# Kernel optimization log

Measured on AMD Instinct MI355X. Metric: run time of the kernel, lower is better.

The kernel has to match this reference:

```python
import jax, jax.numpy as jnp
import numpy as np

NUM_CLASSES = 2
THRESHOLD = 0.5
NEGPOS_RATIO = 3
VAR0, VAR1 = 0.1, 0.2  # self.variance = [0.1, 0.2]


def point_form(priors):
    # [cx,cy,w,h] -> [xmin,ymin,xmax,ymax]
    return jnp.concatenate([priors[:, :2] - priors[:, 2:] / 2,
                            priors[:, :2] + priors[:, 2:] / 2], axis=1)


def jaccard(a, b):
    # a: [O,4], b: [P,4] point-form -> IoU [O,P]
    tl = jnp.maximum(a[:, None, :2], b[None, :, :2])
    br = jnp.minimum(a[:, None, 2:], b[None, :, 2:])
    wh = jnp.clip(br - tl, 0.0)
    inter = wh[..., 0] * wh[..., 1]
    area_a = ((a[:, 2] - a[:, 0]) * (a[:, 3] - a[:, 1]))[:, None]
    area_b = ((b[:, 2] - b[:, 0]) * (b[:, 3] - b[:, 1]))[None, :]
    return inter / (area_a + area_b - inter)


def encode(matched, priors):
    # matched: [P,4] point-form GT, priors: [P,4] center-size
    g_cxcy = ((matched[:, :2] + matched[:, 2:]) / 2 - priors[:, :2]) / (VAR0 * priors[:, 2:])
    g_wh = jnp.log((matched[:, 2:] - matched[:, :2]) / priors[:, 2:]) / VAR1
    return jnp.concatenate([g_cxcy, g_wh], axis=1)


def match_one(truths, labels, priors):
    # truths: [O,4], labels: [O], priors: [P,4]
    O = truths.shape[0]
    overlaps = jaccard(truths, point_form(priors))          # [O,P]
    best_prior_idx = jnp.argmax(overlaps, axis=1)           # [O] best prior per GT
    best_truth_overlap = jnp.max(overlaps, axis=0)          # [P]
    best_truth_idx = jnp.argmax(overlaps, axis=0)           # [P]
    # ensure each GT keeps its best prior
    best_truth_overlap = best_truth_overlap.at[best_prior_idx].set(2.0)
    best_truth_idx = best_truth_idx.at[best_prior_idx].set(jnp.arange(O))
    matches = truths[best_truth_idx]                        # [P,4]
    conf = labels[best_truth_idx].astype(jnp.int32)         # head label == 1
    conf = jnp.where(best_truth_overlap < THRESHOLD, 0, conf)
    loc = encode(matches, priors)                           # [P,4]
    return loc, conf


def setup_inputs() -> dict:
    key = jax.random.key(0)
    k1, k2, k3, k4, k5, k6 = jax.random.split(key, 6)
    B, P, O = 32, 32768, 32
    loc_data = jax.random.normal(k1, (B, P, 3), jnp.float32) * 0.1
    conf_data = jax.random.normal(k2, (B, P, 2), jnp.float32)
    cxy = jax.random.uniform(k3, (P, 2), jnp.float32, 0.1, 0.9)
    wh = jax.random.uniform(k4, (P, 2), jnp.float32, 0.05, 0.2)
    priors = jnp.concatenate([cxy, wh], axis=1)
    xy1 = jax.random.uniform(k5, (B, O, 2), jnp.float32, 0.0, 0.7)
    twh = jax.random.uniform(k6, (B, O, 2), jnp.float32, 0.05, 0.25)
    targets = jnp.concatenate([xy1, xy1 + twh, jnp.ones((B, O, 1), jnp.float32)], axis=2)
    return {"loc_data": loc_data, "conf_data": conf_data, "priors": priors, "targets": targets}


def reference(loc_data, conf_data, priors, targets):
    B, P, _ = loc_data.shape
    # convert_coord: [cx, cy, gw] -> [cx, cy, gw, gw]
    quard = jnp.stack([loc_data[..., 0], loc_data[..., 1],
                       loc_data[..., 2], loc_data[..., 2]], axis=-1)  # [B,P,4]
    truths = targets[..., :4]
    labels = targets[..., 4]
    loc_t, conf_t = jax.vmap(lambda t, l: match_one(t, l, priors))(truths, labels)
    pos = conf_t > 0                                         # [B,P]
    # localization smooth-L1 over positives (sum reduction)
    d = quard - loc_t
    ad = jnp.abs(d)
    sl1 = jnp.where(ad < 1.0, 0.5 * d * d, ad - 0.5)
    loss_l = jnp.sum(sl1 * pos[..., None].astype(sl1.dtype))
    # per-prior CE for hard-negative mining
    lse = jax.nn.logsumexp(conf_data, axis=-1)               # [B,P]
    picked = jnp.take_along_axis(conf_data, conf_t[..., None], axis=-1)[..., 0]
    ce = lse - picked                                        # [B,P]
    ce_mine = jnp.where(pos, 0.0, ce)
    # double argsort -> rank of each prior by mining loss (descending)
    loss_idx = jnp.argsort(-ce_mine, axis=1)
    idx_rank = jnp.argsort(loss_idx, axis=1)
    num_pos = jnp.sum(pos.astype(jnp.int32), axis=1, keepdims=True)  # [B,1]
    num_neg = jnp.minimum(NEGPOS_RATIO * num_pos, P - 1)
    neg = idx_rank < num_neg
    sel = jnp.logical_or(pos, neg)
    loss_c = jnp.sum(jnp.where(sel, ce, 0.0))
    N = jnp.sum(num_pos).astype(loss_l.dtype)
    return loss_l / N, loss_c / N
```

## Files before the change

### kernel.cpp

```cpp
#include <hip/hip_runtime.h>
#include <math.h>

#define Bn 32
#define Pn 32768
#define On 32


__global__ __launch_bounds__(256) void phase1(const float4* __restrict__ priors,
                                              const float* __restrict__ targets,
                                              unsigned long long* __restrict__ bpm,
                                              uchar4* __restrict__ pack) {
    int b = blockIdx.y;
    int base = blockIdx.x * 1024;
    int tid = threadIdx.x;
    int lane = tid & 63, wv = tid >> 6;

    __shared__ float4 tb[On];
    __shared__ float  ta[On];
    __shared__ unsigned long long wred[On][4];

    if (tid < On) {
        const float* t = targets + ((size_t)b * On + tid) * 5;
        float x1 = t[0], y1 = t[1], x2 = t[2], y2 = t[3];
        tb[tid] = make_float4(x1, y1, x2, y2);
        ta[tid] = (x2 - x1) * (y2 - y1);
    }
    __syncthreads();

    int p0 = base + tid * 4;
    float px1[4], py1[4], px2[4], py2[4], ab[4];
#pragma unroll
    for (int j = 0; j < 4; j++) {
        float4 pr = priors[p0 + j];
        px1[j] = pr.x - pr.z * 0.5f; py1[j] = pr.y - pr.w * 0.5f;
        px2[j] = pr.x + pr.z * 0.5f; py2[j] = pr.y + pr.w * 0.5f;
        ab[j]  = (px2[j] - px1[j]) * (py2[j] - py1[j]);
    }

    float bI[4] = {0.f, 0.f, 0.f, 0.f};
    float bU[4] = {1.f, 1.f, 1.f, 1.f};
    int   bx[4] = {0, 0, 0, 0};

    for (int o = 0; o < On; o++) {
        float4 tt = tb[o];
        float  a  = ta[o];
        float I[4], U[4];
#pragma unroll
        for (int j = 0; j < 4; j++) {
            float ix1 = fmaxf(tt.x, px1[j]), iy1 = fmaxf(tt.y, py1[j]);
            float ix2 = fminf(tt.z, px2[j]), iy2 = fminf(tt.w, py2[j]);
            float iw = fmaxf(ix2 - ix1, 0.f), ih = fmaxf(iy2 - iy1, 0.f);
            I[j] = iw * ih;
            U[j] = a + ab[j] - I[j];
            if (I[j] * bU[j] > bI[j] * U[j]) { bI[j] = I[j]; bU[j] = U[j]; bx[j] = o; }
        }
        float cI = I[0], cU = U[0]; int cp = p0;
#pragma unroll
        for (int j = 1; j < 4; j++)
            if (I[j] * cU > cI * U[j]) { cI = I[j]; cU = U[j]; cp = p0 + j; }
        float iou = cI / cU;
        unsigned long long key = ((unsigned long long)__float_as_uint(iou) << 32)
                               | (unsigned)(Pn - 1 - cp);
#pragma unroll
        for (int off = 32; off > 0; off >>= 1) {
            unsigned long long ok = __shfl_down(key, off, 64);
            if (ok > key) key = ok;
        }
        if (lane == 0) wred[o][wv] = key;
    }
    __syncthreads();
    if (tid < On) {
        unsigned long long kk = wred[tid][0];
#pragma unroll
        for (int w = 1; w < 4; w++) if (wred[tid][w] > kk) kk = wred[tid][w];
        atomicMax(&bpm[b * On + tid], kk);
    }

    uchar4 pk;
    pk.x = (unsigned char)(bx[0] | ((bI[0] >= 0.5f * bU[0]) ? 32 : 0));
    pk.y = (unsigned char)(bx[1] | ((bI[1] >= 0.5f * bU[1]) ? 32 : 0));
    pk.z = (unsigned char)(bx[2] | ((bI[2] >= 0.5f * bU[2]) ? 32 : 0));
    pk.w = (unsigned char)(bx[3] | ((bI[3] >= 0.5f * bU[3]) ? 32 : 0));
    pack[(size_t)b * (Pn / 4) + blockIdx.x * 256 + tid] = pk;
}

__global__ __launch_bounds__(256) void phase2(const float* __restrict__ loc,
                                              const float4* __restrict__ conf4,
                                              const float4* __restrict__ priors,
                                              const float* __restrict__ targets,
                                              const unsigned long long* __restrict__ bpm,
                                              const uchar4* __restrict__ pack,
                                              float* __restrict__ ce_mine,
                                              int* __restrict__ num_pos,
                                              float* __restrict__ loss_l_t,
                                              float* __restrict__ ce_t,
                                              int* __restrict__ np_tot) {
    int b = blockIdx.y;
    int base = blockIdx.x * 1024;
    int tid = threadIdx.x;

    __shared__ float4 tb[On];
    __shared__ float  lb[On];
    __shared__ int    forced[1024];
    __shared__ float  sred[12];

    forced[tid] = -1; forced[tid + 256] = -1; forced[tid + 512] = -1; forced[tid + 768] = -1;
    int sp = -1;
    if (tid < On) {
        const float* t = targets + ((size_t)b * On + tid) * 5;
        tb[tid] = make_float4(t[0], t[1], t[2], t[3]);
        lb[tid] = t[4];
        sp = Pn - 1 - (int)(bpm[b * On + tid] & 0xFFFFFFFFull);
    }
    __syncthreads();
    if (tid < On && sp >= base && sp < base + 1024)
        atomicMax(&forced[sp - base], tid);
    __syncthreads();

    int p0 = base + tid * 4;
    uchar4 pk = pack[(size_t)b * (Pn / 4) + blockIdx.x * 256 + tid];
    size_t cb = ((size_t)b * Pn + p0) >> 1;
    float4 cA = conf4[cb], cB = conf4[cb + 1];

    unsigned char pkb[4] = {pk.x, pk.y, pk.z, pk.w};
    float c0a[4] = {cA.x, cA.z, cB.x, cB.z};
    float c1a[4] = {cA.y, cA.w, cB.y, cB.w};
    float cem[4];
    float ll_s = 0.f, pce_s = 0.f, cnt_s = 0.f;

#pragma unroll
    for (int j = 0; j < 4; j++) {
        int fo = forced[tid * 4 + j];
        int bidx = (fo >= 0) ? fo : (pkb[j] & 31);
        int cf = ((fo >= 0) || (pkb[j] & 32)) ? (int)lb[bidx] : 0;
        bool pos = cf > 0;
        if (pos) {
            float4 tt = tb[bidx];
            float4 pr = priors[p0 + j];
            float g0 = ((tt.x + tt.z) * 0.5f - pr.x) / (0.1f * pr.z);
            float g1 = ((tt.y + tt.w) * 0.5f - pr.y) / (0.1f * pr.w);
            float g2 = __logf((tt.z - tt.x) / pr.z) * 5.0f;
            float g3 = __logf((tt.w - tt.y) / pr.w) * 5.0f;
            const float* lp = loc + ((size_t)b * Pn + p0 + j) * 3;
            float q0 = lp[0], q1 = lp[1], q2 = lp[2];
            float dd[4] = { q0 - g0, q1 - g1, q2 - g2, q2 - g3 };
#pragma unroll
            for (int i = 0; i < 4; i++) {
                float ad = fabsf(dd[i]);
                ll_s += (ad < 1.f) ? 0.5f * dd[i] * dd[i] : (ad - 0.5f);
            }
            cnt_s += 1.f;
        }
        float m = fmaxf(c0a[j], c1a[j]);
        float lse = m + __logf(__expf(c0a[j] - m) + __expf(c1a[j] - m));
        float ce = lse - (cf ? c1a[j] : c0a[j]);
        if (pos) { pce_s += ce; ce = 0.f; }
        cem[j] = fmaxf(ce, 0.f);
    }
    ((float4*)ce_mine)[((size_t)b * Pn + p0) >> 2] = make_float4(cem[0], cem[1], cem[2], cem[3]);

#pragma unroll
    for (int off = 32; off > 0; off >>= 1) {
        ll_s  += __shfl_down(ll_s,  off, 64);
        pce_s += __shfl_down(pce_s, off, 64);
        cnt_s += __shfl_down(cnt_s, off, 64);
    }
    int lane = tid & 63, wv = tid >> 6;
    if (lane == 0) { sred[wv*3] = ll_s; sred[wv*3+1] = pce_s; sred[wv*3+2] = cnt_s; }
    __syncthreads();
    if (tid == 0) {
        float llr = 0, pcer = 0, cntr = 0;
        for (int w = 0; w < 4; w++) { llr += sred[w*3]; pcer += sred[w*3+1]; cntr += sred[w*3+2]; }
        if (llr != 0.f)  atomicAdd(loss_l_t, llr);
        if (pcer != 0.f) atomicAdd(ce_t, pcer);
        int c = (int)cntr;
        if (c) { atomicAdd(&num_pos[b], c); atomicAdd(np_tot, c); }
    }
}

__global__ __launch_bounds__(1024) void topk(const float* __restrict__ ce_mine,
                                             const int* __restrict__ num_pos,
                                             float* __restrict__ ce_t) {
    int b = blockIdx.x, tid = threadIdx.x;
    const float4* v4 = (const float4*)(ce_mine + (size_t)b * Pn);
    float4 r[8];
#pragma unroll
    for (int i = 0; i < 8; i++) r[i] = v4[i * 1024 + tid];

    int k = 3 * num_pos[b];
    if (k > Pn - 1) k = Pn - 1;
    if (k <= 0) return;

    __shared__ int   scnt[34];
    __shared__ float ssum[16];
    __shared__ int   sct[16];
    for (int i = tid; i < 34; i += 1024) scnt[i] = 0;
    __syncthreads();

    unsigned lo = 0u, hi = 0x7F800000u;
    int round = 0;
    while (hi - lo > 1u && round < 32) {
        unsigned mid = lo + ((hi - lo) >> 1);
        float mf = __uint_as_float(mid);
        int c = 0;
#pragma unroll
        for (int i = 0; i < 8; i++)
            c += (r[i].x > mf) + (r[i].y > mf) + (r[i].z > mf) + (r[i].w > mf);
#pragma unroll
        for (int off = 32; off > 0; off >>= 1) c += __shfl_down(c, off, 64);
        if ((tid & 63) == 0) atomicAdd(&scnt[round], c);
        __syncthreads();
        int tot = scnt[round];
        round++;
        if (tot == k) { hi = mid; break; }
        if (tot >= k) lo = mid; else hi = mid;
    }

    float tv = __uint_as_float(hi);
    float s = 0.f; int c = 0;
#pragma unroll
    for (int i = 0; i < 8; i++) {
        if (r[i].x > tv) { s += r[i].x; c++; }
        if (r[i].y > tv) { s += r[i].y; c++; }
        if (r[i].z > tv) { s += r[i].z; c++; }
        if (r[i].w > tv) { s += r[i].w; c++; }
    }
#pragma unroll
    for (int off = 32; off > 0; off >>= 1) {
        s += __shfl_down(s, off, 64);
        c += __shfl_down(c, off, 64);
    }
    if ((tid & 63) == 0) { ssum[tid >> 6] = s; sct[tid >> 6] = c; }
    __syncthreads();
    if (tid == 0) {
        float st = 0.f; int ct = 0;
        for (int w = 0; w < 16; w++) { st += ssum[w]; ct += sct[w]; }
        atomicAdd(ce_t, st + (float)(k - ct) * tv);
    }
}

__global__ void finalize(const float* __restrict__ loss_l_t,
                         const float* __restrict__ ce_t,
                         const int* __restrict__ np_tot,
                         float* __restrict__ out) {
    float N = (float)(*np_tot);
    out[0] = *loss_l_t / N;
    out[1] = *ce_t / N;
}

extern "C" void kernel_launch(void* const* d_in, const int* in_sizes, int n_in,
                              void* d_out, int out_size, void* d_ws, size_t ws_size,
                              hipStream_t stream) {
    const float* loc     = (const float*)d_in[0];
    const float* conf    = (const float*)d_in[1];
    const float* priors  = (const float*)d_in[2];
    const float* targets = (const float*)d_in[3];
    float* out = (float*)d_out;

    char* ws = (char*)d_ws;
    unsigned long long* bpm = (unsigned long long*)ws;
    int*   num_pos  = (int*)(ws + 8192);
    float* loss_l_t = (float*)(ws + 8320);
    float* ce_t     = (float*)(ws + 8324);
    int*   np_tot   = (int*)(ws + 8328);
    uchar4* pack    = (uchar4*)(ws + 16384);
    float* ce_mine  = (float*)(ws + 16384 + (size_t)Bn * Pn);

    hipMemsetAsync(ws, 0, 16384, stream);

    hipLaunchKernelGGL(phase1, dim3(Pn / 1024, Bn), dim3(256), 0, stream,
                       (const float4*)priors, targets, bpm, pack);
    hipLaunchKernelGGL(phase2, dim3(Pn / 1024, Bn), dim3(256), 0, stream,
                       loc, (const float4*)conf, (const float4*)priors, targets, bpm, pack,
                       ce_mine, num_pos, loss_l_t, ce_t, np_tot);
    hipLaunchKernelGGL(topk, dim3(Bn), dim3(1024), 0, stream, ce_mine, num_pos, ce_t);
    hipLaunchKernelGGL(finalize, dim3(1), dim3(1), 0, stream, loss_l_t, ce_t, np_tot, out);
}
```

Measured before the change: 175.7 us.

## Fuse all phases into one persistent kernel with grid barriers and histogram top-k

Merges matching, loss computation, hard-negative top-k and finalize into a single 1024-block kernel synchronized by software grid barriers, keeping per-prior best-truth indices in registers instead of a packed global buffer. Each block builds a shared-memory histogram of mining losses over the upper bits of the float value. The top-k stage then uses the merged histogram to find the threshold bin and bisects only over candidates in that bin, instead of running a full 32-round bisection over all priors. It relies on all 1024 blocks being co-resident for the spin barriers and adds shared-memory atomics plus global histogram traffic.

```diff
diff --git a/kernel.cpp b/kernel.cpp
--- a/kernel.cpp
+++ b/kernel.cpp
@@ -4,30 +4,58 @@
 #define Bn 32
 #define Pn 32768
 #define On 32
-
-
-__global__ __launch_bounds__(256) void phase1(const float4* __restrict__ priors,
-                                              const float* __restrict__ targets,
-                                              unsigned long long* __restrict__ bpm,
-                                              uchar4* __restrict__ pack) {
-    int b = blockIdx.y;
-    int base = blockIdx.x * 1024;
-    int tid = threadIdx.x;
-    int lane = tid & 63, wv = tid >> 6;
+#define NBLK 1024
+#define NBINS 2048
+#define CANDCAP 4096
+
+
+__device__ __forceinline__ void gbar(int* ctr, int tid) {
+    __syncthreads();
+    if (tid == 0) {
+        __threadfence();
+        __hip_atomic_fetch_add(ctr, 1, __ATOMIC_RELEASE, __HIP_MEMORY_SCOPE_AGENT);
+        while (__hip_atomic_load(ctr, __ATOMIC_ACQUIRE, __HIP_MEMORY_SCOPE_AGENT) < NBLK)
+            __builtin_amdgcn_s_sleep(1);
+        __threadfence();
+    }
+    __syncthreads();
+}
+
+__global__ __launch_bounds__(256, 4) void fused(
+    const float* __restrict__ loc, const float4* __restrict__ conf4,
+    const float4* __restrict__ priors, const float* __restrict__ targets,
+    unsigned long long* __restrict__ bpm, int* __restrict__ num_pos,
+    float* __restrict__ loss_l_t, float* __restrict__ ce_t,
+    int* __restrict__ np_tot, int* __restrict__ bar, int* __restrict__ hist,
+    float* __restrict__ ce_mine, float* __restrict__ out)
+{
+    const int bid = blockIdx.x;
+    const int c = bid & 31, b = bid >> 5;
+    const int tid = threadIdx.x;
+    const int lane = tid & 63, wv = tid >> 6;
 
     __shared__ float4 tb[On];
-    __shared__ float  ta[On];
+    __shared__ float  ta_lb[On];
     __shared__ unsigned long long wred[On][4];
+    __shared__ int    forced[1024];
+    __shared__ float  sred[12];
+    __shared__ int    shist[NBINS];
+    __shared__ float  cand[CANDCAP];
+    __shared__ int    s3i[4];
+    __shared__ float  s3f[2];
+    __shared__ int    ired[4];
+    __shared__ float  fred[4];
 
     if (tid < On) {
         const float* t = targets + ((size_t)b * On + tid) * 5;
         float x1 = t[0], y1 = t[1], x2 = t[2], y2 = t[3];
         tb[tid] = make_float4(x1, y1, x2, y2);
-        ta[tid] = (x2 - x1) * (y2 - y1);
-    }
-    __syncthreads();
-
-    int p0 = base + tid * 4;
+        ta_lb[tid] = (x2 - x1) * (y2 - y1);
+    }
+    __syncthreads();
+
+    const int base = c * 1024;
+    const int p0 = base + tid * 4;
     float px1[4], py1[4], px2[4], py2[4], ab[4];
 #pragma unroll
     for (int j = 0; j < 4; j++) {
@@ -36,14 +64,13 @@
         px2[j] = pr.x + pr.z * 0.5f; py2[j] = pr.y + pr.w * 0.5f;
         ab[j]  = (px2[j] - px1[j]) * (py2[j] - py1[j]);
     }
-
     float bI[4] = {0.f, 0.f, 0.f, 0.f};
     float bU[4] = {1.f, 1.f, 1.f, 1.f};
     int   bx[4] = {0, 0, 0, 0};
 
     for (int o = 0; o < On; o++) {
         float4 tt = tb[o];
-        float  a  = ta[o];
+        float  a  = ta_lb[o];
         float I[4], U[4];
 #pragma unroll
         for (int j = 0; j < 4; j++) {
@@ -75,41 +102,18 @@
         for (int w = 1; w < 4; w++) if (wred[tid][w] > kk) kk = wred[tid][w];
         atomicMax(&bpm[b * On + tid], kk);
     }
-
-    uchar4 pk;
-    pk.x = (unsigned char)(bx[0] | ((bI[0] >= 0.5f * bU[0]) ? 32 : 0));
-    pk.y = (unsigned char)(bx[1] | ((bI[1] >= 0.5f * bU[1]) ? 32 : 0));
-    pk.z = (unsigned char)(bx[2] | ((bI[2] >= 0.5f * bU[2]) ? 32 : 0));
-    pk.w = (unsigned char)(bx[3] | ((bI[3] >= 0.5f * bU[3]) ? 32 : 0));
-    pack[(size_t)b * (Pn / 4) + blockIdx.x * 256 + tid] = pk;
-}
-
-__global__ __launch_bounds__(256) void phase2(const float* __restrict__ loc,
-                                              const float4* __restrict__ conf4,
-                                              const float4* __restrict__ priors,
-                                              const float* __restrict__ targets,
-                                              const unsigned long long* __restrict__ bpm,
-                                              const uchar4* __restrict__ pack,
-                                              float* __restrict__ ce_mine,
-                                              int* __restrict__ num_pos,
-                                              float* __restrict__ loss_l_t,
-                                              float* __restrict__ ce_t,
-                                              int* __restrict__ np_tot) {
-    int b = blockIdx.y;
-    int base = blockIdx.x * 1024;
-    int tid = threadIdx.x;
-
-    __shared__ float4 tb[On];
-    __shared__ float  lb[On];
-    __shared__ int    forced[1024];
-    __shared__ float  sred[12];
+    int flags = 0;
+#pragma unroll
+    for (int j = 0; j < 4; j++) if (bI[j] >= 0.5f * bU[j]) flags |= 1 << j;
+
+    gbar(&bar[0], tid);
 
     forced[tid] = -1; forced[tid + 256] = -1; forced[tid + 512] = -1; forced[tid + 768] = -1;
+    int* lhist = (int*)cand;
+    for (int i = tid; i < NBINS; i += 256) lhist[i] = 0;
     int sp = -1;
     if (tid < On) {
-        const float* t = targets + ((size_t)b * On + tid) * 5;
-        tb[tid] = make_float4(t[0], t[1], t[2], t[3]);
-        lb[tid] = t[4];
+        ta_lb[tid] = targets[((size_t)b * On + tid) * 5 + 4];
         sp = Pn - 1 - (int)(bpm[b * On + tid] & 0xFFFFFFFFull);
     }
     __syncthreads();
@@ -117,12 +121,8 @@
         atomicMax(&forced[sp - base], tid);
     __syncthreads();
 
-    int p0 = base + tid * 4;
-    uchar4 pk = pack[(size_t)b * (Pn / 4) + blockIdx.x * 256 + tid];
     size_t cb = ((size_t)b * Pn + p0) >> 1;
     float4 cA = conf4[cb], cB = conf4[cb + 1];
-
-    unsigned char pkb[4] = {pk.x, pk.y, pk.z, pk.w};
     float c0a[4] = {cA.x, cA.z, cB.x, cB.z};
     float c1a[4] = {cA.y, cA.w, cB.y, cB.w};
     float cem[4];
@@ -131,8 +131,8 @@
 #pragma unroll
     for (int j = 0; j < 4; j++) {
         int fo = forced[tid * 4 + j];
-        int bidx = (fo >= 0) ? fo : (pkb[j] & 31);
-        int cf = ((fo >= 0) || (pkb[j] & 32)) ? (int)lb[bidx] : 0;
+        int bidx = (fo >= 0) ? fo : bx[j];
+        int cf = ((fo >= 0) || ((flags >> j) & 1)) ? (int)ta_lb[bidx] : 0;
         bool pos = cf > 0;
         if (pos) {
             float4 tt = tb[bidx];
@@ -156,6 +156,7 @@
         float ce = lse - (cf ? c1a[j] : c0a[j]);
         if (pos) { pce_s += ce; ce = 0.f; }
         cem[j] = fmaxf(ce, 0.f);
+        atomicAdd(&lhist[__float_as_uint(cem[j]) >> 20], 1);
     }
     ((float4*)ce_mine)[((size_t)b * Pn + p0) >> 2] = make_float4(cem[0], cem[1], cem[2], cem[3]);
 
@@ -165,7 +166,6 @@
         pce_s += __shfl_down(pce_s, off, 64);
         cnt_s += __shfl_down(cnt_s, off, 64);
     }
-    int lane = tid & 63, wv = tid >> 6;
     if (lane == 0) { sred[wv*3] = ll_s; sred[wv*3+1] = pce_s; sred[wv*3+2] = cnt_s; }
     __syncthreads();
     if (tid == 0) {
@@ -173,88 +173,164 @@
         for (int w = 0; w < 4; w++) { llr += sred[w*3]; pcer += sred[w*3+1]; cntr += sred[w*3+2]; }
         if (llr != 0.f)  atomicAdd(loss_l_t, llr);
         if (pcer != 0.f) atomicAdd(ce_t, pcer);
-        int c = (int)cntr;
-        if (c) { atomicAdd(&num_pos[b], c); atomicAdd(np_tot, c); }
-    }
-}
-
-__global__ __launch_bounds__(1024) void topk(const float* __restrict__ ce_mine,
-                                             const int* __restrict__ num_pos,
-                                             float* __restrict__ ce_t) {
-    int b = blockIdx.x, tid = threadIdx.x;
-    const float4* v4 = (const float4*)(ce_mine + (size_t)b * Pn);
-    float4 r[8];
-#pragma unroll
-    for (int i = 0; i < 8; i++) r[i] = v4[i * 1024 + tid];
-
-    int k = 3 * num_pos[b];
-    if (k > Pn - 1) k = Pn - 1;
-    if (k <= 0) return;
-
-    __shared__ int   scnt[34];
-    __shared__ float ssum[16];
-    __shared__ int   sct[16];
-    for (int i = tid; i < 34; i += 1024) scnt[i] = 0;
-    __syncthreads();
-
-    unsigned lo = 0u, hi = 0x7F800000u;
-    int round = 0;
-    while (hi - lo > 1u && round < 32) {
-        unsigned mid = lo + ((hi - lo) >> 1);
-        float mf = __uint_as_float(mid);
-        int c = 0;
-#pragma unroll
-        for (int i = 0; i < 8; i++)
-            c += (r[i].x > mf) + (r[i].y > mf) + (r[i].z > mf) + (r[i].w > mf);
-#pragma unroll
-        for (int off = 32; off > 0; off >>= 1) c += __shfl_down(c, off, 64);
-        if ((tid & 63) == 0) atomicAdd(&scnt[round], c);
-        __syncthreads();
-        int tot = scnt[round];
-        round++;
-        if (tot == k) { hi = mid; break; }
-        if (tot >= k) lo = mid; else hi = mid;
-    }
-
-    float tv = __uint_as_float(hi);
-    float s = 0.f; int c = 0;
-#pragma unroll
-    for (int i = 0; i < 8; i++) {
-        if (r[i].x > tv) { s += r[i].x; c++; }
-        if (r[i].y > tv) { s += r[i].y; c++; }
-        if (r[i].z > tv) { s += r[i].z; c++; }
-        if (r[i].w > tv) { s += r[i].w; c++; }
-    }
-#pragma unroll
-    for (int off = 32; off > 0; off >>= 1) {
-        s += __shfl_down(s, off, 64);
-        c += __shfl_down(c, off, 64);
-    }
-    if ((tid & 63) == 0) { ssum[tid >> 6] = s; sct[tid >> 6] = c; }
+        int cc = (int)cntr;
+        if (cc) { atomicAdd(&num_pos[b], cc); atomicAdd(np_tot, cc); }
+    }
+    for (int i = tid; i < NBINS; i += 256) {
+        int v = lhist[i];
+        if (v) atomicAdd(&hist[b * NBINS + i], v);
+    }
+
+    gbar(&bar[1], tid);
+
+    if (bid < Bn) {
+        int b3 = bid;
+        int k = 3 * num_pos[b3];
+        if (k > Pn - 1) k = Pn - 1;
+        if (k > 0) {
+            const int* gh = hist + b3 * NBINS;
+            for (int i = tid; i < NBINS; i += 256) shist[i] = gh[i];
+            __syncthreads();
+            int ps = 0;
+#pragma unroll
+            for (int i = 0; i < 8; i++) ps += shist[tid * 8 + i];
+            forced[tid] = ps;
+            __syncthreads();
+            if (tid == 0) {
+                int cacc = 0, m = 0, cab = 0;
+                for (int t = 255; t >= 0; t--) {
+                    if (cacc + forced[t] >= k) {
+                        for (int i = t * 8 + 7; i >= t * 8; i--) {
+                            if (cacc + shist[i] >= k) { m = i; cab = cacc; break; }
+                            cacc += shist[i];
+                        }
+                        break;
+                    }
+                    cacc += forced[t];
+                }
+                s3i[0] = m; s3i[1] = cab; s3i[2] = 0;
+            }
+            __syncthreads();
+            const int m = s3i[0], cab = s3i[1], kk = k - cab;
+            const int cntm = shist[m];
+            const float4* v4 = (const float4*)(ce_mine + (size_t)b3 * Pn);
+
+            if (cntm <= CANDCAP) {
+                float shi = 0.f;
+                for (int i = 0; i < 32; i++) {
+                    float4 r = v4[i * 256 + tid];
+                    float vv[4] = {r.x, r.y, r.z, r.w};
+#pragma unroll
+                    for (int q = 0; q < 4; q++) {
+                        int kb = (int)(__float_as_uint(vv[q]) >> 20);
+                        if (kb > m) shi += vv[q];
+                        else if (kb == m) cand[atomicAdd(&s3i[2], 1)] = vv[q];
+                    }
+                }
+#pragma unroll
+                for (int off = 32; off > 0; off >>= 1) shi += __shfl_down(shi, off, 64);
+                if (lane == 0) fred[wv] = shi;
+                __syncthreads();
+                if (tid == 0) s3f[0] = fred[0] + fred[1] + fred[2] + fred[3];
+                int n = s3i[2];
+                unsigned lo = (unsigned)m << 20, hi = ((unsigned)m + 1u) << 20;
+                __syncthreads();
+                while (hi - lo > 1u) {
+                    unsigned mid = lo + ((hi - lo) >> 1);
+                    float mf = __uint_as_float(mid);
+                    int ccc = 0;
+                    for (int i = tid; i < n; i += 256) ccc += (cand[i] > mf);
+#pragma unroll
+                    for (int off = 32; off > 0; off >>= 1) ccc += __shfl_down(ccc, off, 64);
+                    if (lane == 0) ired[wv] = ccc;
+                    __syncthreads();
+                    int tot = ired[0] + ired[1] + ired[2] + ired[3];
+                    __syncthreads();
+                    if (tot == kk) { hi = mid; break; }
+                    if (tot >= kk) lo = mid; else hi = mid;
+                }
+                float tv = __uint_as_float(hi);
+                float s = 0.f; int ct = 0;
+                for (int i = tid; i < n; i += 256) {
+                    float v = cand[i];
+                    if (v > tv) { s += v; ct++; }
+                }
+#pragma unroll
+                for (int off = 32; off > 0; off >>= 1) {
+                    s += __shfl_down(s, off, 64); ct += __shfl_down(ct, off, 64);
+                }
+                if (lane == 0) { fred[wv] = s; ired[wv] = ct; }
+                __syncthreads();
+                if (tid == 0) {
+                    float st = fred[0] + fred[1] + fred[2] + fred[3];
+                    int ctt = ired[0] + ired[1] + ired[2] + ired[3];
+                    atomicAdd(ce_t, s3f[0] + st + (float)(kk - ctt) * tv);
+                }
+            } else {
+                unsigned lo = (unsigned)m << 20, hi = ((unsigned)m + 1u) << 20;
+                while (hi - lo > 1u) {
+                    unsigned mid = lo + ((hi - lo) >> 1);
+                    float mf = __uint_as_float(mid);
+                    int ccc = 0;
+                    for (int i = 0; i < 32; i++) {
+                        float4 r = v4[i * 256 + tid];
+                        ccc += (r.x > mf) + (r.y > mf) + (r.z > mf) + (r.w > mf);
+                    }
+#pragma unroll
+                    for (int off = 32; off > 0; off >>= 1) ccc += __shfl_down(ccc, off, 64);
+                    if (lane == 0) ired[wv] = ccc;
+                    __syncthreads();
+                    int tot = ired[0] + ired[1] + ired[2] + ired[3];
+                    __syncthreads();
+                    if (tot == k) { hi = mid; break; }
+                    if (tot >= k) lo = mid; else hi = mid;
+                }
+                float tv = __uint_as_float(hi);
+                float s = 0.f; int ct = 0;
+                for (int i = 0; i < 32; i++) {
+                    float4 r = v4[i * 256 + tid];
+                    if (r.x > tv) { s += r.x; ct++; }
+                    if (r.y > tv) { s += r.y; ct++; }
+                    if (r.z > tv) { s += r.z; ct++; }
+                    if (r.w > tv) { s += r.w; ct++; }
+                }
+#pragma unroll
+                for (int off = 32; off > 0; off >>= 1) {
+                    s += __shfl_down(s, off, 64); ct += __shfl_down(ct, off, 64);
+                }
+                if (lane == 0) { fred[wv] = s; ired[wv] = ct; }
+                __syncthreads();
+                if (tid == 0) {
+                    float st = fred[0] + fred[1] + fred[2] + fred[3];
+                    int ctt = ired[0] + ired[1] + ired[2] + ired[3];
+                    atomicAdd(ce_t, st + (float)(k - ctt) * tv);
+                }
+            }
+        }
+    }
+
     __syncthreads();
     if (tid == 0) {
-        float st = 0.f; int ct = 0;
-        for (int w = 0; w < 16; w++) { st += ssum[w]; ct += sct[w]; }
-        atomicAdd(ce_t, st + (float)(k - ct) * tv);
-    }
-}
-
-__global__ void finalize(const float* __restrict__ loss_l_t,
-                         const float* __restrict__ ce_t,
-                         const int* __restrict__ np_tot,
-                         float* __restrict__ out) {
-    float N = (float)(*np_tot);
-    out[0] = *loss_l_t / N;
-    out[1] = *ce_t / N;
+        __threadfence();
+        __hip_atomic_fetch_add(&bar[2], 1, __ATOMIC_RELEASE, __HIP_MEMORY_SCOPE_AGENT);
+        if (bid == 0) {
+            while (__hip_atomic_load(&bar[2], __ATOMIC_ACQUIRE, __HIP_MEMORY_SCOPE_AGENT) < NBLK)
+                __builtin_amdgcn_s_sleep(1);
+            __threadfence();
+            float N = (float)(*np_tot);
+            out[0] = *loss_l_t / N;
+            out[1] = *ce_t / N;
+        }
+    }
 }
 
 extern "C" void kernel_launch(void* const* d_in, const int* in_sizes, int n_in,
                               void* d_out, int out_size, void* d_ws, size_t ws_size,
                               hipStream_t stream) {
-    const float* loc     = (const float*)d_in[0];
-    const float* conf    = (const float*)d_in[1];
-    const float* priors  = (const float*)d_in[2];
-    const float* targets = (const float*)d_in[3];
+    const float*  loc     = (const float*)d_in[0];
+    const float4* conf4   = (const float4*)d_in[1];
+    const float4* priors  = (const float4*)d_in[2];
+    const float*  targets = (const float*)d_in[3];
     float* out = (float*)d_out;
 
     char* ws = (char*)d_ws;
@@ -263,16 +339,13 @@
     float* loss_l_t = (float*)(ws + 8320);
     float* ce_t     = (float*)(ws + 8324);
     int*   np_tot   = (int*)(ws + 8328);
-    uchar4* pack    = (uchar4*)(ws + 16384);
-    float* ce_mine  = (float*)(ws + 16384 + (size_t)Bn * Pn);
-
-    hipMemsetAsync(ws, 0, 16384, stream);
-
-    hipLaunchKernelGGL(phase1, dim3(Pn / 1024, Bn), dim3(256), 0, stream,
-                       (const float4*)priors, targets, bpm, pack);
-    hipLaunchKernelGGL(phase2, dim3(Pn / 1024, Bn), dim3(256), 0, stream,
-                       loc, (const float4*)conf, (const float4*)priors, targets, bpm, pack,
-                       ce_mine, num_pos, loss_l_t, ce_t, np_tot);
-    hipLaunchKernelGGL(topk, dim3(Bn), dim3(1024), 0, stream, ce_mine, num_pos, ce_t);
-    hipLaunchKernelGGL(finalize, dim3(1), dim3(1), 0, stream, loss_l_t, ce_t, np_tot, out);
+    int*   bar      = (int*)(ws + 8336);
+    int*   hist     = (int*)(ws + 16384);
+    float* ce_mine  = (float*)(ws + 16384 + (size_t)Bn * NBINS * 4);
+
+    hipMemsetAsync(ws, 0, 16384 + (size_t)Bn * NBINS * 4, stream);
+
+    hipLaunchKernelGGL(fused, dim3(NBLK), dim3(256), 0, stream,
+                       loc, conf4, priors, targets, bpm, num_pos,
+                       loss_l_t, ce_t, np_tot, bar, hist, ce_mine, out);
 }
```

After: 437.6 us. 149% more time.
